# Kernel tuning notes

Measured on AMD Instinct MI355X. Metric: run time of the kernel, lower is better.

Reference implementation:

```python
import jax, jax.numpy as jnp
import numpy as np

B, L, D, H = 1, 4096, 512, 8
HD = D // H  # head_dim = 64


def _relative_bias(rel, length):
    # rel: [H, 2L] learnable; returns [H, L, L] relative position bias
    h = rel.shape[0]
    r = jnp.tile(rel, (1, length))                      # [H, 2L*L]
    r = r[:, : length * (2 * length - 1)]
    r = r.reshape(h, length, 2 * length - 1)
    return r[..., length - 1:]                          # [H, L, L]


def setup_inputs() -> dict:
    key = jax.random.key(0)
    ks = jax.random.split(key, 12)
    std = D ** -0.5
    inp = {
        "x": jax.random.normal(ks[0], (B, L, D), jnp.float32),
        "pos_embed": jax.random.normal(ks[1], (L, D), jnp.float32) * std,
        "rel_bias": jnp.zeros((H, 2 * L), jnp.float32) + 0.01 * jax.random.normal(ks[2], (H, 2 * L), jnp.float32),
        "Wq": jax.random.normal(ks[3], (D, H, HD), jnp.float32) * std,
        "bq": jnp.zeros((H, HD), jnp.float32),
        "Wk": jax.random.normal(ks[4], (D, H, HD), jnp.float32) * std,
        "bk": jnp.zeros((H, HD), jnp.float32),
        "Wv": jax.random.normal(ks[5], (D, H, HD), jnp.float32) * std,
        "bv": jnp.zeros((H, HD), jnp.float32),
        "Wo": jax.random.normal(ks[6], (H, HD, D), jnp.float32) * (D ** -0.5),
        "bo": jnp.zeros((D,), jnp.float32),
    }
    return inp


def reference(x, pos_embed, rel_bias, Wq, bq, Wk, bk, Wv, bv, Wo, bo):
    # Positional embedding
    x = x + pos_embed
    # QKV projections: [B, L, H, HD]
    q = jnp.einsum("bld,dhk->blhk", x, Wq) + bq
    k = jnp.einsum("bld,dhk->blhk", x, Wk) + bk
    v = jnp.einsum("bld,dhk->blhk", x, Wv) + bv
    # Scaled dot-product attention with relative attention bias
    depth = q.shape[-1]
    q = q / jnp.sqrt(jnp.asarray(depth, q.dtype))
    scores = jnp.einsum("bqhd,bkhd->bhqk", q, k)       # [B, H, L, L]
    bias = _relative_bias(rel_bias, x.shape[1])         # [H, L, L]
    scores = scores + bias[None]
    attn = jax.nn.softmax(scores, axis=-1)
    out = jnp.einsum("bhqk,bkhd->bqhd", attn, v)       # [B, L, H, HD]
    # Output projection back to D
    return jnp.einsum("bqhd,hdD->bqD", out, Wo) + bo
```

## Files before the change

kernel.cpp:

```cpp
#include <hip/hip_runtime.h>
#include <hip/hip_bf16.h>


typedef __attribute__((ext_vector_type(8))) short bf16x8;
typedef __attribute__((ext_vector_type(4))) short bf16x4;
typedef __attribute__((ext_vector_type(4))) float f32x4;
typedef __attribute__((ext_vector_type(2))) unsigned u32x2;

__device__ __forceinline__ short f2bf(float f) {
    unsigned u = __builtin_bit_cast(unsigned, f);
    u += 0x7fff + ((u >> 16) & 1);
    return (short)(u >> 16);
}

__device__ __forceinline__ float bf2f(short s) {
    unsigned u = ((unsigned)(unsigned short)s) << 16;
    return __builtin_bit_cast(float, u);
}

__device__ __forceinline__ f32x4 mfma32(bf16x8 a, bf16x8 b, f32x4 c) {
    return __builtin_amdgcn_mfma_f32_16x16x32_bf16(a, b, c, 0, 0, 0);
}

__device__ __forceinline__ unsigned cvtpk(float a, float b) {
    unsigned r;
    asm("v_cvt_pk_bf16_f32 %0, %1, %2" : "=v"(r) : "v"(a), "v"(b));
    return r;
}

__device__ __forceinline__ void gll16(const short* src, short* ldsdst) {
    __builtin_amdgcn_global_load_lds(
        (const __attribute__((address_space(1))) unsigned*)src,
        (__attribute__((address_space(3))) unsigned*)ldsdst, 16, 0, 0);
}

__global__ __launch_bounds__(256) void k_prep_xp(const float* __restrict__ x,
                                                 const float* __restrict__ pos,
                                                 short* __restrict__ xp) {
    int i = (blockIdx.x * 256 + threadIdx.x) * 8;
    float4 a0 = *(const float4*)(x + i);
    float4 a1 = *(const float4*)(x + i + 4);
    float4 b0 = *(const float4*)(pos + i);
    float4 b1 = *(const float4*)(pos + i + 4);
    bf16x8 v;
    v[0] = f2bf(a0.x + b0.x); v[1] = f2bf(a0.y + b0.y);
    v[2] = f2bf(a0.z + b0.z); v[3] = f2bf(a0.w + b0.w);
    v[4] = f2bf(a1.x + b1.x); v[5] = f2bf(a1.y + b1.y);
    v[6] = f2bf(a1.z + b1.z); v[7] = f2bf(a1.w + b1.w);
    *(bf16x8*)(xp + i) = v;
}

__global__ __launch_bounds__(256) void k_prep_wqkv(const float* __restrict__ Wq,
                                                   const float* __restrict__ Wk,
                                                   const float* __restrict__ Wv,
                                                   short* __restrict__ WT) {
    int idx = blockIdx.x * 256 + threadIdx.x;
    int n = idx >> 9, k = idx & 511;
    int nn = n & 511;
    const float* src = (n < 512) ? Wq : (n < 1024 ? Wk : Wv);
    float scale = (n < 512) ? 0.125f : 1.0f;
    WT[idx] = f2bf(src[k * 512 + nn] * scale);
}

__global__ __launch_bounds__(256) void k_prep_wo(const float* __restrict__ Wo,
                                                 short* __restrict__ WoT) {
    int idx = blockIdx.x * 256 + threadIdx.x;
    int n = idx >> 9, k = idx & 511;
    WoT[idx] = f2bf(Wo[k * 512 + n]);
}

__global__ __launch_bounds__(256) void k_vt(const short* __restrict__ Vg,
                                            short* __restrict__ VT) {
    __shared__ short tile[64][72];
    const int tid = threadIdx.x;
    const int h = blockIdx.y, kvb = blockIdx.x * 64;
    const short* src = Vg + (size_t)h * 4096 * 64;
    short* dst = VT + (size_t)h * 64 * 4096;
    #pragma unroll
    for (int i = 0; i < 2; ++i) {
        int ch = tid + 256 * i;
        int r = ch >> 3, c = (ch & 7) * 8;
        *(uint4*)&tile[r][c] = *(const uint4*)(src + (size_t)(kvb + r) * 64 + c);
    }
    __syncthreads();
    #pragma unroll
    for (int i = 0; i < 2; ++i) {
        int ch = tid + 256 * i;
        int d = ch >> 3, kc = (ch & 7) * 8;
        bf16x8 v;
        #pragma unroll
        for (int j = 0; j < 8; ++j) v[j] = tile[kc + j][d];
        *(bf16x8*)(dst + (size_t)d * 4096 + kvb + kc) = v;
    }
}

template <int MODE>
__global__ __launch_bounds__(256) void k_gemm(const short* __restrict__ A,
                                              const short* __restrict__ Bt,
                                              const float* __restrict__ bias0,
                                              const float* __restrict__ bias1,
                                              const float* __restrict__ bias2,
                                              short* __restrict__ Qg,
                                              short* __restrict__ Kg,
                                              short* __restrict__ Vg,
                                              float* __restrict__ Cout) {
    __shared__ short Al[128][72];
    __shared__ short Bl[128][72];
    const int tid = threadIdx.x;
    const int lane = tid & 63, wid = tid >> 6;
    const int wm = wid >> 1, wn = wid & 1;
    const int mb = blockIdx.y * 128, nb = blockIdx.x * 128;
    const int lr = lane & 15, lg = lane >> 4;

    f32x4 acc[4][4] = {};

    for (int kk = 0; kk < 512; kk += 64) {
        #pragma unroll
        for (int i = 0; i < 4; ++i) {
            int o = tid + 256 * i;
            int row = o >> 3, c8 = (o & 7) * 8;
            *(uint4*)(&Al[row][c8]) = *(const uint4*)(A + (size_t)(mb + row) * 512 + kk + c8);
            *(uint4*)(&Bl[row][c8]) = *(const uint4*)(Bt + (size_t)(nb + row) * 512 + kk + c8);
        }
        __syncthreads();
        #pragma unroll
        for (int ks = 0; ks < 2; ++ks) {
            bf16x8 af[4], bfr[4];
            #pragma unroll
            for (int t = 0; t < 4; ++t) {
                af[t]  = *(const bf16x8*)(&Al[wm * 64 + t * 16 + lr][ks * 32 + lg * 8]);
                bfr[t] = *(const bf16x8*)(&Bl[wn * 64 + t * 16 + lr][ks * 32 + lg * 8]);
            }
            #pragma unroll
            for (int mt = 0; mt < 4; ++mt)
                #pragma unroll
                for (int nt = 0; nt < 4; ++nt)
                    acc[mt][nt] = mfma32(af[mt], bfr[nt], acc[mt][nt]);
        }
        __syncthreads();
    }

    #pragma unroll
    for (int mt = 0; mt < 4; ++mt) {
        #pragma unroll
        for (int nt = 0; nt < 4; ++nt) {
            #pragma unroll
            for (int r = 0; r < 4; ++r) {
                int m = mb + wm * 64 + mt * 16 + lg * 4 + r;
                int n = nb + wn * 64 + nt * 16 + lr;
                float v = acc[mt][nt][r];
                if (MODE == 0) {
                    int which = n >> 9;
                    int nn = n & 511;
                    int hh = nn >> 6, hd = nn & 63;
                    const float* bp = (which == 0) ? bias0 : (which == 1 ? bias1 : bias2);
                    v += bp[nn] * (which == 0 ? 0.125f : 1.0f);
                    short* dst = (which == 0) ? Qg : (which == 1 ? Kg : Vg);
                    dst[((size_t)hh * 4096 + m) * 64 + hd] = f2bf(v);
                } else {
                    Cout[(size_t)m * 512 + n] = v + bias0[n];
                }
            }
        }
    }
}

__global__ __launch_bounds__(512, 1) void k_attn2(const short* __restrict__ Qg,
                                                  const short* __restrict__ Kg,
                                                  const short* __restrict__ VT,
                                                  const float* __restrict__ rel,
                                                  short* __restrict__ AO) {
    __shared__ __align__(16) char smem[157952];
    short* KlB = (short*)smem;
    short* VsB = (short*)(smem + 65536);
    short* biaslh = (short*)(smem + 149504);

    const int tid = threadIdx.x;
    const int lane = tid & 63, wq = tid >> 6;
    const int lr = lane & 15, lg = lane >> 4;
    const int g = wq & 1, sp = wq >> 1;
    const int h = blockIdx.y;
    const int qb = blockIdx.x * 128;

    short* Pw = (short*)(smem + 131072 + wq * 2304);

    const short* Qh = Qg + (size_t)h * 4096 * 64;
    const short* Kh = Kg + (size_t)h * 4096 * 64;
    const short* VTh = VT + (size_t)h * 64 * 4096;
    const float* relh = rel + h * 8192;

    int koffE[4], voffE[4];
    #pragma unroll
    for (int i = 0; i < 4; ++i) {
        int ch = g * 256 + i * 64 + lane;
        int row = ch >> 3, kc = ch & 7;
        koffE[i] = row * 64 + (kc ^ (row & 7)) * 8;
        voffE[i] = row * 4096 + (kc ^ (row & 7)) * 8;
    }

    bf16x8 qf[4][2];
    #pragma unroll
    for (int qt = 0; qt < 4; ++qt)
        #pragma unroll
        for (int dk = 0; dk < 2; ++dk)
            qf[qt][dk] = *(const bf16x8*)(Qh + (size_t)(qb + g * 64 + qt * 16 + lr) * 64 + dk * 32 + lg * 8);

    for (int j = tid; j < 4224; j += 512) biaslh[j] = f2bf(relh[3968 - qb + j]);

    const int kvbase = sp * 1024;

    {
        const short* ks = Kh + (size_t)kvbase * 64;
        const short* vs = VTh + kvbase;
        short* kd = KlB + sp * 4096;
        short* vd = VsB + sp * 4096;
        #pragma unroll
        for (int i = 0; i < 4; ++i) {
            gll16(ks + koffE[i], kd + (g * 256 + i * 64) * 8);
            gll16(vs + voffE[i], vd + (g * 256 + i * 64) * 8);
        }
    }
    __syncthreads();

    f32x4 acc[4][4] = {};
    float lsum[4] = {0.f, 0.f, 0.f, 0.f};
    const float L2E = 1.4426950408889634f;

    #pragma unroll 1
    for (int it = 0; it < 16; ++it) {
        const int buf = it & 1;
        if (it + 1 < 16) {
            const short* ks = Kh + (size_t)(kvbase + (it + 1) * 64) * 64;
            const short* vs = VTh + kvbase + (it + 1) * 64;
            short* kd = KlB + ((buf ^ 1) * 4 + sp) * 4096;
            short* vd = VsB + ((buf ^ 1) * 4 + sp) * 4096;
            #pragma unroll
            for (int i = 0; i < 4; ++i) {
                gll16(ks + koffE[i], kd + (g * 256 + i * 64) * 8);
                gll16(vs + voffE[i], vd + (g * 256 + i * 64) * 8);
            }
        }

        const short* Kt = KlB + (buf * 4 + sp) * 4096;
        const char*  Vtb = (const char*)(VsB + (buf * 4 + sp) * 4096);

        float bwL[7][4];
        {
            int jb = kvbase + it * 64 + 127 + lg * 4 - g * 64 - lr - 48;
            #pragma unroll
            for (int gi = 0; gi < 7; ++gi)
                #pragma unroll
                for (int r = 0; r < 4; ++r)
                    bwL[gi][r] = bf2f(biaslh[jb + gi * 16 + r]) * L2E;
        }

        bf16x8 kf[4][2];
        #pragma unroll
        for (int t = 0; t < 4; ++t) {
            kf[t][0] = *(const bf16x8*)(Kt + (t * 16 + lr) * 64 + ((lg) ^ (lr & 7)) * 8);
            kf[t][1] = *(const bf16x8*)(Kt + (t * 16 + lr) * 64 + ((4 + lg) ^ (lr & 7)) * 8);
        }
        bf16x8 vf[4][2];
        #pragma unroll
        for (int dt = 0; dt < 4; ++dt)
            #pragma unroll
            for (int w = 0; w < 2; ++w)
                vf[dt][w] = *(const bf16x8*)(Vtb + (dt * 16 + lr) * 128 + (((w * 4 + lg) ^ (lr & 7)) << 4));

        #pragma unroll
        for (int qt = 0; qt < 4; ++qt) {
            f32x4 sv[4];
            #pragma unroll
            for (int t = 0; t < 4; ++t) {
                f32x4 z = {0.f, 0.f, 0.f, 0.f};
                z = mfma32(kf[t][0], qf[qt][0], z);
                z = mfma32(kf[t][1], qf[qt][1], z);
                sv[t] = z;
            }

            asm volatile("s_waitcnt lgkmcnt(0)" ::: "memory");
            __builtin_amdgcn_sched_barrier(0);

            #pragma unroll
            for (int t = 0; t < 4; ++t) {
                float p0 = exp2f(fmaf(sv[t][0], L2E, bwL[t - qt + 3][0]));
                float p1 = exp2f(fmaf(sv[t][1], L2E, bwL[t - qt + 3][1]));
                float p2 = exp2f(fmaf(sv[t][2], L2E, bwL[t - qt + 3][2]));
                float p3 = exp2f(fmaf(sv[t][3], L2E, bwL[t - qt + 3][3]));
                lsum[qt] += (p0 + p1) + (p2 + p3);
                u32x2 pk;
                pk[0] = cvtpk(p0, p1);
                pk[1] = cvtpk(p2, p3);
                *(u32x2*)(Pw + lr * 72 + t * 16 + lg * 4) = pk;
            }
            __builtin_amdgcn_sched_barrier(0);

            bf16x8 pb0 = *(const bf16x8*)(Pw + lr * 72 + lg * 8);
            bf16x8 pb1 = *(const bf16x8*)(Pw + lr * 72 + 32 + lg * 8);

            #pragma unroll
            for (int dt = 0; dt < 4; ++dt) {
                acc[qt][dt] = mfma32(vf[dt][0], pb0, acc[qt][dt]);
                acc[qt][dt] = mfma32(vf[dt][1], pb1, acc[qt][dt]);
            }
        }
        __syncthreads();
    }

    #pragma unroll
    for (int qt = 0; qt < 4; ++qt) {
        float v = lsum[qt];
        v += __shfl_xor(v, 16);
        v += __shfl_xor(v, 32);
        lsum[qt] = v;
    }

    float* Opart = (float*)smem;
    float* Lpart = (float*)(smem + 139264);
    #pragma unroll
    for (int qt = 0; qt < 4; ++qt) {
        #pragma unroll
        for (int dt = 0; dt < 4; ++dt)
            *(f32x4*)&Opart[(((g * 4 + sp) * 4 + qt) * 16 + lr) * 68 + dt * 16 + lg * 4] = acc[qt][dt];
        if (lg == 0) Lpart[((g * 4 + sp) * 4 + qt) * 16 + lr] = lsum[qt];
    }
    __builtin_amdgcn_sched_barrier(0);
    __syncthreads();
    __builtin_amdgcn_sched_barrier(0);
    {
        const int g2 = tid >> 8, qi = (tid >> 4) & 15, d4 = (tid & 15) * 4;
        #pragma unroll
        for (int qt = 0; qt < 4; ++qt) {
            f32x4 s = {0.f, 0.f, 0.f, 0.f};
            float lt = 0.f;
            #pragma unroll
            for (int s2 = 0; s2 < 4; ++s2) {
                s += *(const f32x4*)&Opart[(((g2 * 4 + s2) * 4 + qt) * 16 + qi) * 68 + d4];
                lt += Lpart[((g2 * 4 + s2) * 4 + qt) * 16 + qi];
            }
            float inv = 1.0f / lt;
            bf16x4 o;
            o[0] = f2bf(s[0] * inv); o[1] = f2bf(s[1] * inv);
            o[2] = f2bf(s[2] * inv); o[3] = f2bf(s[3] * inv);
            int q = qb + g2 * 64 + qt * 16 + qi;
            *(bf16x4*)(AO + (size_t)q * 512 + h * 64 + d4) = o;
        }
    }
}

extern "C" void kernel_launch(void* const* d_in, const int* in_sizes, int n_in,
                              void* d_out, int out_size, void* d_ws, size_t ws_size,
                              hipStream_t stream) {
    const float* x   = (const float*)d_in[0];
    const float* pos = (const float*)d_in[1];
    const float* rel = (const float*)d_in[2];
    const float* Wq  = (const float*)d_in[3];
    const float* bq  = (const float*)d_in[4];
    const float* Wk  = (const float*)d_in[5];
    const float* bk  = (const float*)d_in[6];
    const float* Wv  = (const float*)d_in[7];
    const float* bv  = (const float*)d_in[8];
    const float* Wo  = (const float*)d_in[9];
    const float* bo  = (const float*)d_in[10];
    float* out = (float*)d_out;

    char* ws = (char*)d_ws;
    short* xp    = (short*)ws;  ws += (size_t)4096 * 512 * 2;
    short* WqkvT = (short*)ws;  ws += (size_t)1536 * 512 * 2;
    short* WoT   = (short*)ws;  ws += (size_t)512 * 512 * 2;
    short* Qg    = (short*)ws;  ws += (size_t)8 * 4096 * 64 * 2;
    short* Kg    = (short*)ws;  ws += (size_t)8 * 4096 * 64 * 2;
    short* Vg    = (short*)ws;  ws += (size_t)8 * 4096 * 64 * 2;
    short* AO    = (short*)ws;  ws += (size_t)4096 * 512 * 2;
    short* VT    = xp;

    k_prep_xp<<<dim3(4096 * 512 / (256 * 8)), 256, 0, stream>>>(x, pos, xp);
    k_prep_wqkv<<<dim3(1536 * 512 / 256), 256, 0, stream>>>(Wq, Wk, Wv, WqkvT);
    k_prep_wo<<<dim3(512 * 512 / 256), 256, 0, stream>>>(Wo, WoT);

    k_gemm<0><<<dim3(12, 32), 256, 0, stream>>>(xp, WqkvT, bq, bk, bv, Qg, Kg, Vg, nullptr);
    k_vt<<<dim3(64, 8), 256, 0, stream>>>(Vg, VT);
    k_attn2<<<dim3(32, 8), 512, 0, stream>>>(Qg, Kg, VT, rel, AO);
    k_gemm<1><<<dim3(4, 32), 256, 0, stream>>>(AO, WoT, bo, nullptr, nullptr,
                                               nullptr, nullptr, nullptr, out);
}
```

Before: 135.9 us.

## Rework attention kernel: direct global K/V loads, bias folded into MFMA, MFMA row sums

Replaces the LDS double-buffered K/V staging with direct global-to-register loads per wave. Blocks shrink to 256 threads covering 64 queries, with two blocks per CU across a flat 512-block grid. The log2e factor is folded into the Q weights and a prescaled fp32 relative bias, and that bias is fed as the MFMA accumulator input. Row sums now come from an MFMA against a ones vector instead of VALU adds and shuffles. This removes per-iteration barriers and bias conversion work, but relies on L2 and cache hits for repeated K/V reads and adds a small prep kernel.

```diff
diff --git a/kernel.cpp b/kernel.cpp
--- a/kernel.cpp
+++ b/kernel.cpp
@@ -7,17 +7,14 @@
 typedef __attribute__((ext_vector_type(4))) float f32x4;
 typedef __attribute__((ext_vector_type(2))) unsigned u32x2;
 
+#define QSCALE (0.125f * 1.4426950408889634f)
+
 __device__ __forceinline__ short f2bf(float f) {
     unsigned u = __builtin_bit_cast(unsigned, f);
     u += 0x7fff + ((u >> 16) & 1);
     return (short)(u >> 16);
 }
 
-__device__ __forceinline__ float bf2f(short s) {
-    unsigned u = ((unsigned)(unsigned short)s) << 16;
-    return __builtin_bit_cast(float, u);
-}
-
 __device__ __forceinline__ f32x4 mfma32(bf16x8 a, bf16x8 b, f32x4 c) {
     return __builtin_amdgcn_mfma_f32_16x16x32_bf16(a, b, c, 0, 0, 0);
 }
@@ -26,12 +23,6 @@
     unsigned r;
     asm("v_cvt_pk_bf16_f32 %0, %1, %2" : "=v"(r) : "v"(a), "v"(b));
     return r;
-}
-
-__device__ __forceinline__ void gll16(const short* src, short* ldsdst) {
-    __builtin_amdgcn_global_load_lds(
-        (const __attribute__((address_space(1))) unsigned*)src,
-        (__attribute__((address_space(3))) unsigned*)ldsdst, 16, 0, 0);
 }
 
 __global__ __launch_bounds__(256) void k_prep_xp(const float* __restrict__ x,
@@ -58,7 +49,7 @@
     int n = idx >> 9, k = idx & 511;
     int nn = n & 511;
     const float* src = (n < 512) ? Wq : (n < 1024 ? Wk : Wv);
-    float scale = (n < 512) ? 0.125f : 1.0f;
+    float scale = (n < 512) ? QSCALE : 1.0f;
     WT[idx] = f2bf(src[k * 512 + nn] * scale);
 }
 
@@ -67,6 +58,12 @@
     int idx = blockIdx.x * 256 + threadIdx.x;
     int n = idx >> 9, k = idx & 511;
     WoT[idx] = f2bf(Wo[k * 512 + n]);
+}
+
+__global__ __launch_bounds__(256) void k_prep_rel2(const float* __restrict__ rel,
+                                                   float* __restrict__ rel2) {
+    int i = blockIdx.x * 256 + threadIdx.x;
+    rel2[i] = rel[i] * 1.4426950408889634f;
 }
 
 __global__ __launch_bounds__(256) void k_vt(const short* __restrict__ Vg,
@@ -154,7 +151,7 @@
                     int nn = n & 511;
                     int hh = nn >> 6, hd = nn & 63;
                     const float* bp = (which == 0) ? bias0 : (which == 1 ? bias1 : bias2);
-                    v += bp[nn] * (which == 0 ? 0.125f : 1.0f);
+                    v += bp[nn] * (which == 0 ? QSCALE : 1.0f);
                     short* dst = (which == 0) ? Qg : (which == 1 ? Kg : Vg);
                     dst[((size_t)hh * 4096 + m) * 64 + hd] = f2bf(v);
                 } else {
@@ -165,138 +162,95 @@
     }
 }
 
-__global__ __launch_bounds__(512, 1) void k_attn2(const short* __restrict__ Qg,
+__global__ __launch_bounds__(256, 2) void k_attn3(const short* __restrict__ Qg,
                                                   const short* __restrict__ Kg,
                                                   const short* __restrict__ VT,
-                                                  const float* __restrict__ rel,
+                                                  const float* __restrict__ rel2,
                                                   short* __restrict__ AO) {
-    __shared__ __align__(16) char smem[157952];
-    short* KlB = (short*)smem;
-    short* VsB = (short*)(smem + 65536);
-    short* biaslh = (short*)(smem + 149504);
+    __shared__ __align__(16) char smem[70656];
 
     const int tid = threadIdx.x;
-    const int lane = tid & 63, wq = tid >> 6;
+    const int lane = tid & 63, sp = tid >> 6;
     const int lr = lane & 15, lg = lane >> 4;
-    const int g = wq & 1, sp = wq >> 1;
-    const int h = blockIdx.y;
-    const int qb = blockIdx.x * 128;
-
-    short* Pw = (short*)(smem + 131072 + wq * 2304);
+    const int bid = blockIdx.x;
+    const int h = bid & 7;
+    const int qb = (bid >> 3) * 64;
+
+    short* Pw = (short*)smem + sp * 1152;
 
     const short* Qh = Qg + (size_t)h * 4096 * 64;
     const short* Kh = Kg + (size_t)h * 4096 * 64;
     const short* VTh = VT + (size_t)h * 64 * 4096;
-    const float* relh = rel + h * 8192;
-
-    int koffE[4], voffE[4];
-    #pragma unroll
-    for (int i = 0; i < 4; ++i) {
-        int ch = g * 256 + i * 64 + lane;
-        int row = ch >> 3, kc = ch & 7;
-        koffE[i] = row * 64 + (kc ^ (row & 7)) * 8;
-        voffE[i] = row * 4096 + (kc ^ (row & 7)) * 8;
-    }
 
     bf16x8 qf[4][2];
     #pragma unroll
     for (int qt = 0; qt < 4; ++qt)
         #pragma unroll
         for (int dk = 0; dk < 2; ++dk)
-            qf[qt][dk] = *(const bf16x8*)(Qh + (size_t)(qb + g * 64 + qt * 16 + lr) * 64 + dk * 32 + lg * 8);
-
-    for (int j = tid; j < 4224; j += 512) biaslh[j] = f2bf(relh[3968 - qb + j]);
+            qf[qt][dk] = *(const bf16x8*)(Qh + (size_t)(qb + qt * 16 + lr) * 64 + dk * 32 + lg * 8);
 
     const int kvbase = sp * 1024;
-
-    {
-        const short* ks = Kh + (size_t)kvbase * 64;
-        const short* vs = VTh + kvbase;
-        short* kd = KlB + sp * 4096;
-        short* vd = VsB + sp * 4096;
-        #pragma unroll
-        for (int i = 0; i < 4; ++i) {
-            gll16(ks + koffE[i], kd + (g * 256 + i * 64) * 8);
-            gll16(vs + voffE[i], vd + (g * 256 + i * 64) * 8);
-        }
-    }
-    __syncthreads();
+    const short* kp = Kh + (size_t)kvbase * 64;
+    const short* vp = VTh + kvbase;
+    const float* bp = rel2 + h * 8192 + (kvbase + 4095 - qb) + lg * 4 - lr;
 
     f32x4 acc[4][4] = {};
-    float lsum[4] = {0.f, 0.f, 0.f, 0.f};
-    const float L2E = 1.4426950408889634f;
+    f32x4 lacc[4] = {};
+
+    bf16x8 ones;
+    #pragma unroll
+    for (int i = 0; i < 8; ++i) ones[i] = (short)0x3F80;
 
     #pragma unroll 1
     for (int it = 0; it < 16; ++it) {
-        const int buf = it & 1;
-        if (it + 1 < 16) {
-            const short* ks = Kh + (size_t)(kvbase + (it + 1) * 64) * 64;
-            const short* vs = VTh + kvbase + (it + 1) * 64;
-            short* kd = KlB + ((buf ^ 1) * 4 + sp) * 4096;
-            short* vd = VsB + ((buf ^ 1) * 4 + sp) * 4096;
-            #pragma unroll
-            for (int i = 0; i < 4; ++i) {
-                gll16(ks + koffE[i], kd + (g * 256 + i * 64) * 8);
-                gll16(vs + voffE[i], vd + (g * 256 + i * 64) * 8);
-            }
-        }
-
-        const short* Kt = KlB + (buf * 4 + sp) * 4096;
-        const char*  Vtb = (const char*)(VsB + (buf * 4 + sp) * 4096);
-
-        float bwL[7][4];
-        {
-            int jb = kvbase + it * 64 + 127 + lg * 4 - g * 64 - lr - 48;
-            #pragma unroll
-            for (int gi = 0; gi < 7; ++gi)
+        bf16x8 kf[4][2];
+        #pragma unroll
+        for (int t = 0; t < 4; ++t) {
+            kf[t][0] = *(const bf16x8*)(kp + (size_t)(t * 16 + lr) * 64 + lg * 8);
+            kf[t][1] = *(const bf16x8*)(kp + (size_t)(t * 16 + lr) * 64 + 32 + lg * 8);
+        }
+        bf16x8 vf[4][2];
+        #pragma unroll
+        for (int dt = 0; dt < 4; ++dt)
+            #pragma unroll
+            for (int w = 0; w < 2; ++w)
+                vf[dt][w] = *(const bf16x8*)(vp + (size_t)(dt * 16 + lr) * 4096 + w * 32 + lg * 8);
+
+        #pragma unroll
+        for (int qt = 0; qt < 4; ++qt) {
+            f32x4 cin[4];
+            #pragma unroll
+            for (int t = 0; t < 4; ++t)
                 #pragma unroll
                 for (int r = 0; r < 4; ++r)
-                    bwL[gi][r] = bf2f(biaslh[jb + gi * 16 + r]) * L2E;
-        }
-
-        bf16x8 kf[4][2];
-        #pragma unroll
-        for (int t = 0; t < 4; ++t) {
-            kf[t][0] = *(const bf16x8*)(Kt + (t * 16 + lr) * 64 + ((lg) ^ (lr & 7)) * 8);
-            kf[t][1] = *(const bf16x8*)(Kt + (t * 16 + lr) * 64 + ((4 + lg) ^ (lr & 7)) * 8);
-        }
-        bf16x8 vf[4][2];
-        #pragma unroll
-        for (int dt = 0; dt < 4; ++dt)
-            #pragma unroll
-            for (int w = 0; w < 2; ++w)
-                vf[dt][w] = *(const bf16x8*)(Vtb + (dt * 16 + lr) * 128 + (((w * 4 + lg) ^ (lr & 7)) << 4));
-
-        #pragma unroll
-        for (int qt = 0; qt < 4; ++qt) {
-            f32x4 sv[4];
+                    cin[t][r] = bp[(t - qt) * 16 + r];
+
+            unsigned pk0[4], pk1[4];
             #pragma unroll
             for (int t = 0; t < 4; ++t) {
-                f32x4 z = {0.f, 0.f, 0.f, 0.f};
-                z = mfma32(kf[t][0], qf[qt][0], z);
+                f32x4 z = mfma32(kf[t][0], qf[qt][0], cin[t]);
                 z = mfma32(kf[t][1], qf[qt][1], z);
-                sv[t] = z;
+                float p0 = exp2f(z[0]), p1 = exp2f(z[1]);
+                float p2 = exp2f(z[2]), p3 = exp2f(z[3]);
+                pk0[t] = cvtpk(p0, p1);
+                pk1[t] = cvtpk(p2, p3);
             }
 
             asm volatile("s_waitcnt lgkmcnt(0)" ::: "memory");
             __builtin_amdgcn_sched_barrier(0);
-
             #pragma unroll
             for (int t = 0; t < 4; ++t) {
-                float p0 = exp2f(fmaf(sv[t][0], L2E, bwL[t - qt + 3][0]));
-                float p1 = exp2f(fmaf(sv[t][1], L2E, bwL[t - qt + 3][1]));
-                float p2 = exp2f(fmaf(sv[t][2], L2E, bwL[t - qt + 3][2]));
-                float p3 = exp2f(fmaf(sv[t][3], L2E, bwL[t - qt + 3][3]));
-                lsum[qt] += (p0 + p1) + (p2 + p3);
                 u32x2 pk;
-                pk[0] = cvtpk(p0, p1);
-                pk[1] = cvtpk(p2, p3);
+                pk[0] = pk0[t]; pk[1] = pk1[t];
                 *(u32x2*)(Pw + lr * 72 + t * 16 + lg * 4) = pk;
             }
             __builtin_amdgcn_sched_barrier(0);
 
             bf16x8 pb0 = *(const bf16x8*)(Pw + lr * 72 + lg * 8);
             bf16x8 pb1 = *(const bf16x8*)(Pw + lr * 72 + 32 + lg * 8);
+
+            lacc[qt] = mfma32(ones, pb0, lacc[qt]);
+            lacc[qt] = mfma32(ones, pb1, lacc[qt]);
 
             #pragma unroll
             for (int dt = 0; dt < 4; ++dt) {
@@ -304,47 +258,54 @@
                 acc[qt][dt] = mfma32(vf[dt][1], pb1, acc[qt][dt]);
             }
         }
-        __syncthreads();
-    }
-
+        kp += 64 * 64;
+        vp += 64;
+        bp += 64;
+    }
+
+    __builtin_amdgcn_sched_barrier(0);
+    __syncthreads();
+    __builtin_amdgcn_sched_barrier(0);
+
+    float* Opart = (float*)smem;
+    float* Lpart = (float*)(smem + 69632);
     #pragma unroll
     for (int qt = 0; qt < 4; ++qt) {
-        float v = lsum[qt];
-        v += __shfl_xor(v, 16);
-        v += __shfl_xor(v, 32);
-        lsum[qt] = v;
-    }
-
-    float* Opart = (float*)smem;
-    float* Lpart = (float*)(smem + 139264);
-    #pragma unroll
-    for (int qt = 0; qt < 4; ++qt) {
         #pragma unroll
         for (int dt = 0; dt < 4; ++dt)
-            *(f32x4*)&Opart[(((g * 4 + sp) * 4 + qt) * 16 + lr) * 68 + dt * 16 + lg * 4] = acc[qt][dt];
-        if (lg == 0) Lpart[((g * 4 + sp) * 4 + qt) * 16 + lr] = lsum[qt];
+            *(f32x4*)&Opart[((sp * 4 + qt) * 16 + lr) * 68 + dt * 16 + lg * 4] = acc[qt][dt];
+        if (lg == 0) Lpart[(sp * 4 + qt) * 16 + lr] = lacc[qt][0];
     }
     __builtin_amdgcn_sched_barrier(0);
     __syncthreads();
     __builtin_amdgcn_sched_barrier(0);
     {
-        const int g2 = tid >> 8, qi = (tid >> 4) & 15, d4 = (tid & 15) * 4;
-        #pragma unroll
-        for (int qt = 0; qt < 4; ++qt) {
-            f32x4 s = {0.f, 0.f, 0.f, 0.f};
-            float lt = 0.f;
-            #pragma unroll
-            for (int s2 = 0; s2 < 4; ++s2) {
-                s += *(const f32x4*)&Opart[(((g2 * 4 + s2) * 4 + qt) * 16 + qi) * 68 + d4];
-                lt += Lpart[((g2 * 4 + s2) * 4 + qt) * 16 + qi];
-            }
-            float inv = 1.0f / lt;
-            bf16x4 o;
-            o[0] = f2bf(s[0] * inv); o[1] = f2bf(s[1] * inv);
-            o[2] = f2bf(s[2] * inv); o[3] = f2bf(s[3] * inv);
-            int q = qb + g2 * 64 + qt * 16 + qi;
-            *(bf16x4*)(AO + (size_t)q * 512 + h * 64 + d4) = o;
-        }
+        const int qi = tid >> 2, quad = tid & 3;
+        const int qt2 = qi >> 4, qr = qi & 15;
+        f32x4 s0 = {}, s1 = {}, s2 = {}, s3 = {};
+        float lt = 0.f;
+        #pragma unroll
+        for (int s = 0; s < 4; ++s) {
+            const float* o = &Opart[((s * 4 + qt2) * 16 + qr) * 68 + quad * 16];
+            s0 += *(const f32x4*)(o + 0);
+            s1 += *(const f32x4*)(o + 4);
+            s2 += *(const f32x4*)(o + 8);
+            s3 += *(const f32x4*)(o + 12);
+            lt += Lpart[(s * 4 + qt2) * 16 + qr];
+        }
+        float inv = 1.0f / lt;
+        bf16x8 o0, o1;
+        o0[0] = f2bf(s0[0] * inv); o0[1] = f2bf(s0[1] * inv);
+        o0[2] = f2bf(s0[2] * inv); o0[3] = f2bf(s0[3] * inv);
+        o0[4] = f2bf(s1[0] * inv); o0[5] = f2bf(s1[1] * inv);
+        o0[6] = f2bf(s1[2] * inv); o0[7] = f2bf(s1[3] * inv);
+        o1[0] = f2bf(s2[0] * inv); o1[1] = f2bf(s2[1] * inv);
+        o1[2] = f2bf(s2[2] * inv); o1[3] = f2bf(s2[3] * inv);
+        o1[4] = f2bf(s3[0] * inv); o1[5] = f2bf(s3[1] * inv);
+        o1[6] = f2bf(s3[2] * inv); o1[7] = f2bf(s3[3] * inv);
+        short* dst = AO + (size_t)(qb + qi) * 512 + h * 64 + quad * 16;
+        *(bf16x8*)(dst) = o0;
+        *(bf16x8*)(dst + 8) = o1;
     }
 }
 
@@ -372,15 +333,17 @@
     short* Kg    = (short*)ws;  ws += (size_t)8 * 4096 * 64 * 2;
     short* Vg    = (short*)ws;  ws += (size_t)8 * 4096 * 64 * 2;
     short* AO    = (short*)ws;  ws += (size_t)4096 * 512 * 2;
+    float* rel2  = (float*)ws;  ws += (size_t)8 * 8192 * 4;
     short* VT    = xp;
 
     k_prep_xp<<<dim3(4096 * 512 / (256 * 8)), 256, 0, stream>>>(x, pos, xp);
     k_prep_wqkv<<<dim3(1536 * 512 / 256), 256, 0, stream>>>(Wq, Wk, Wv, WqkvT);
     k_prep_wo<<<dim3(512 * 512 / 256), 256, 0, stream>>>(Wo, WoT);
+    k_prep_rel2<<<dim3(8 * 8192 / 256), 256, 0, stream>>>(rel, rel2);
 
     k_gemm<0><<<dim3(12, 32), 256, 0, stream>>>(xp, WqkvT, bq, bk, bv, Qg, Kg, Vg, nullptr);
     k_vt<<<dim3(64, 8), 256, 0, stream>>>(Vg, VT);
-    k_attn2<<<dim3(32, 8), 512, 0, stream>>>(Qg, Kg, VT, rel, AO);
+    k_attn3<<<dim3(512), 256, 0, stream>>>(Qg, Kg, VT, rel2, AO);
     k_gemm<1><<<dim3(4, 32), 256, 0, stream>>>(AO, WoT, bo, nullptr, nullptr,
                                                nullptr, nullptr, nullptr, out);
 }
```

Result: faster. 130.0 us (-4.3%).
